# Kernel optimization log

Measured on AMD Instinct MI355X. Metric: run time of the kernel, lower is better.

Reference implementation:

```python
import jax, jax.numpy as jnp
import numpy as np

E = 8   # num_experts
K = 2   # experts per token


def setup_inputs() -> dict:
    key = jax.random.key(0)
    k1, k2, k3, k4 = jax.random.split(key, 4)
    B, S, H, F = 8, 2048, 1024, 2048
    x = jax.random.normal(k1, (B, S, H), jnp.float32)
    Wg = jax.random.normal(k2, (H, E), jnp.float32) * 0.02
    W1 = jax.random.normal(k3, (E, H, F), jnp.float32) * 0.02
    W2 = jax.random.normal(k4, (E, F, H), jnp.float32) * 0.02
    return {"x": x, "Wg": Wg, "W1": W1, "W2": W2}


def reference(x, Wg, W1, W2):
    orig_shape = x.shape
    xt = x.reshape(-1, orig_shape[-1])          # [T, H]
    T = xt.shape[0]

    # router (no jitter noise: training=False path)
    router_logits = xt @ Wg                     # [T, E]
    routing_weights = jax.nn.softmax(router_logits, axis=-1)
    expert_weights, expert_indices = jax.lax.top_k(routing_weights, K)  # [T, K]

    # router z-loss (float32, as in source)
    log_z = jax.nn.logsumexp(router_logits.astype(jnp.float32), axis=-1)
    z_loss = jnp.sum(log_z * log_z) / T

    # load-balancing loss, faithful to source: num_experts taken from
    # router_probs.shape[-1] == K, and one_hot(expert_indices, K)
    # (out-of-range indices -> zero rows under jax.nn.one_hot semantics)
    oh_k = jax.nn.one_hot(expert_indices, K, dtype=jnp.float32)  # [T, K, K]
    expert_mask = jnp.max(oh_k, axis=-2)                          # [T, K]
    tokens_per_expert = jnp.mean(expert_mask, axis=0)             # [K]
    router_prob_per_expert = jnp.mean(expert_weights.astype(jnp.float32), axis=0)  # [K]
    aux_loss = jnp.mean(tokens_per_expert * router_prob_per_expert) * (K ** 2)

    # combine weight per (token, expert): sum of top-k weights routed to e
    cw = jnp.einsum('tk,tke->te', expert_weights,
                    jax.nn.one_hot(expert_indices, E, dtype=expert_weights.dtype))  # [T, E]

    # per-expert MLP, weighted combine (loop over small fixed E)
    out = jnp.zeros_like(xt)
    for e in range(E):
        h = jax.nn.gelu(xt @ W1[e], approximate=False)  # [T, F]
        out = out + cw[:, e:e + 1] * (h @ W2[e])        # [T, H]

    return out.reshape(orig_shape), z_loss, aux_loss
```

## Files before the change

kernel.cpp:

```cpp
#include <hip/hip_runtime.h>
#include <math.h>

#define T_TOKENS 16384
#define H_DIM 1024
#define F_DIM 2048
#define E_NUM 8
#define TPR 72
#define TOT_T (2 * TPR)
#define MAX_PAIRS (TOT_T * 256)

typedef __attribute__((ext_vector_type(8))) short bf16x8;
typedef __attribute__((ext_vector_type(4))) float f32x4;
typedef __attribute__((ext_vector_type(4))) unsigned short us4;

struct TopK { int e0, e1; float w0, w1; };

__device__ __forceinline__ unsigned short f2bf(float f) {
  unsigned int u = __float_as_uint(f);
  u = (u + 0x7fffu + ((u >> 16) & 1u)) >> 16;
  return (unsigned short)u;
}

__device__ __forceinline__ float bf2f(unsigned short u) {
  return __uint_as_float(((unsigned int)u) << 16);
}

__device__ __forceinline__ void gload_lds16(const void* g, void* l) {
  __builtin_amdgcn_global_load_lds(
      (const __attribute__((address_space(1))) void*)g,
      (__attribute__((address_space(3))) void*)l, 16, 0, 0);
}

__global__ __launch_bounds__(256) void transpose_cast(
    const float* __restrict__ in, unsigned short* __restrict__ out, int R, int C) {
  __shared__ float tile[64][65];
  int e = blockIdx.z;
  int r0 = blockIdx.y * 64, c0 = blockIdx.x * 64;
  int tid = threadIdx.x;
  const float* src = in + ((size_t)e * R + r0) * C + c0;
#pragma unroll
  for (int p = 0; p < 4; p++) {
    int id = p * 256 + tid;
    int row = id >> 4, c4 = (id & 15) * 4;
    float4 v = *(const float4*)&src[(size_t)row * C + c4];
    tile[row][c4 + 0] = v.x; tile[row][c4 + 1] = v.y;
    tile[row][c4 + 2] = v.z; tile[row][c4 + 3] = v.w;
  }
  __syncthreads();
  unsigned short* dst = out + ((size_t)e * C + c0) * R + r0;
#pragma unroll
  for (int p = 0; p < 4; p++) {
    int id = p * 256 + tid;
    int c = id >> 4, r4 = (id & 15) * 4;
    us4 pk;
#pragma unroll
    for (int j = 0; j < 4; j++) pk[j] = f2bf(tile[r4 + j][c]);
    *(us4*)&dst[(size_t)c * R + r4] = pk;
  }
}

__global__ __launch_bounds__(256) void prep_kernel(
    const float* __restrict__ x, const float* __restrict__ Wg,
    const float* __restrict__ W1, unsigned short* __restrict__ xb,
    unsigned short* __restrict__ w1t, TopK* __restrict__ topk,
    int* __restrict__ counts, float* __restrict__ scal) {
  __shared__ __align__(16) char shraw[E_NUM * H_DIM * 4 + 256];
  int bid = blockIdx.x;
  int tid = threadIdx.x;
  if (bid >= 1024) {
    float* tile = (float*)shraw;
    int lb = bid - 1024;
    int bx = lb & 31, by = (lb >> 5) & 15, e = lb >> 9;
    int r0 = by * 64, c0 = bx * 64;
    const float* src = W1 + ((size_t)e * H_DIM + r0) * F_DIM + c0;
#pragma unroll
    for (int p = 0; p < 4; p++) {
      int id = p * 256 + tid;
      int row = id >> 4, c4 = (id & 15) * 4;
      float4 v = *(const float4*)&src[(size_t)row * F_DIM + c4];
      tile[row * 65 + c4 + 0] = v.x; tile[row * 65 + c4 + 1] = v.y;
      tile[row * 65 + c4 + 2] = v.z; tile[row * 65 + c4 + 3] = v.w;
    }
    __syncthreads();
    unsigned short* dst = w1t + ((size_t)e * F_DIM + c0) * H_DIM + r0;
#pragma unroll
    for (int p = 0; p < 4; p++) {
      int id = p * 256 + tid;
      int c = id >> 4, r4 = (id & 15) * 4;
      us4 pk;
#pragma unroll
      for (int j = 0; j < 4; j++) pk[j] = f2bf(tile[(r4 + j) * 65 + c]);
      *(us4*)&dst[(size_t)c * H_DIM + r4] = pk;
    }
    return;
  }
  float (*wg)[H_DIM] = (float(*)[H_DIM])shraw;
  int* cnt = (int*)(shraw + E_NUM * H_DIM * 4);
  float (*sred)[5] = (float(*)[5])(shraw + E_NUM * H_DIM * 4 + 64);
  if (tid < 16) cnt[tid] = 0;
  for (int i = tid; i < E_NUM * H_DIM; i += 256) wg[i & 7][i >> 3] = Wg[i];
  __syncthreads();
  int lane = tid & 63, wid = tid >> 6;
  float zacc = 0.f, c0 = 0.f, c1 = 0.f, s0 = 0.f, s1 = 0.f;
  int wgid = bid * 4 + wid;
#pragma unroll
  for (int it = 0; it < 4; ++it) {
    int t = wgid + it * 4096;
    const float4* xr = (const float4*)(x + (size_t)t * H_DIM);
    us4* xbr = (us4*)(xb + (size_t)t * H_DIM);
    float l[E_NUM];
#pragma unroll
    for (int e = 0; e < E_NUM; e++) l[e] = 0.f;
#pragma unroll
    for (int i = 0; i < 4; i++) {
      int j = i * 64 + lane;
      float4 v = xr[j];
      us4 pk;
      pk[0] = f2bf(v.x); pk[1] = f2bf(v.y); pk[2] = f2bf(v.z); pk[3] = f2bf(v.w);
      xbr[j] = pk;
      int h = j * 4;
#pragma unroll
      for (int e = 0; e < E_NUM; e++) {
        const f32x4 wv = *(const f32x4*)&wg[e][h];
        l[e] = fmaf(v.x, wv[0], l[e]);
        l[e] = fmaf(v.y, wv[1], l[e]);
        l[e] = fmaf(v.z, wv[2], l[e]);
        l[e] = fmaf(v.w, wv[3], l[e]);
      }
    }
#pragma unroll
    for (int off = 32; off > 0; off >>= 1) {
#pragma unroll
      for (int e = 0; e < E_NUM; e++) l[e] += __shfl_xor(l[e], off, 64);
    }
    if (lane == 0) {
      float mx = l[0];
#pragma unroll
      for (int e = 1; e < E_NUM; e++) mx = fmaxf(mx, l[e]);
      float p[E_NUM]; float se = 0.f;
#pragma unroll
      for (int e = 0; e < E_NUM; e++) { p[e] = expf(l[e] - mx); se += p[e]; }
      float logz = logf(se) + mx;
      int e0 = 0; float b0 = p[0];
#pragma unroll
      for (int e = 1; e < E_NUM; e++) if (p[e] > b0) { b0 = p[e]; e0 = e; }
      int e1 = -1; float b1 = -1.f;
#pragma unroll
      for (int e = 0; e < E_NUM; e++) if (e != e0 && p[e] > b1) { b1 = p[e]; e1 = e; }
      float w0 = b0 / se, w1 = b1 / se;
      TopK tk; tk.e0 = e0; tk.e1 = e1; tk.w0 = w0; tk.w1 = w1;
      topk[t] = tk;
      atomicAdd(&cnt[e0], 1);
      atomicAdd(&cnt[8 + e1], 1);
      zacc += logz * logz;
      c0 += (e0 == 0 || e1 == 0) ? 1.f : 0.f;
      c1 += (e0 == 1 || e1 == 1) ? 1.f : 0.f;
      s0 += w0; s1 += w1;
    }
  }
  if (lane == 0) {
    sred[wid][0] = zacc; sred[wid][1] = c0; sred[wid][2] = c1;
    sred[wid][3] = s0;   sred[wid][4] = s1;
  }
  __syncthreads();
  if (tid == 0) {
    float a[5] = {0.f, 0.f, 0.f, 0.f, 0.f};
    for (int w2 = 0; w2 < 4; w2++)
      for (int k = 0; k < 5; k++) a[k] += sred[w2][k];
    for (int k = 0; k < 5; k++) atomicAdd(&scal[k], a[k]);
  }
  if (tid < 16 && cnt[tid]) atomicAdd(&counts[tid], cnt[tid]);
}

__global__ __launch_bounds__(256) void scan_kernel(
    const int* __restrict__ counts, int* __restrict__ po,
    int* __restrict__ tile_expert) {
  __shared__ int nt[16], start[16];
  int tid = threadIdx.x;
  if (tid < 16) {
    int r = tid >> 3, e = tid & 7;
    int s = 0;
    for (int j = 0; j < e; j++) s += (counts[(r << 3) + j] + 255) >> 8;
    nt[tid] = (counts[tid] + 255) >> 8;
    start[tid] = s;
    po[tid] = r * TPR * 256 + (s << 8);
  }
  __syncthreads();
  for (int ti = tid; ti < TOT_T; ti += 256) {
    int r = ti / TPR, local = ti % TPR;
    int ex = -1;
#pragma unroll
    for (int e = 0; e < E_NUM; e++) {
      int k = (r << 3) + e;
      if (local >= start[k] && local < start[k] + nt[k]) ex = e;
    }
    tile_expert[ti] = ex;
  }
}

__global__ __launch_bounds__(256) void assign_kernel(
    const TopK* __restrict__ topk, const int* __restrict__ po,
    int* __restrict__ cursors, int* __restrict__ pair_token,
    float* __restrict__ pair_w, int* __restrict__ inv0, int* __restrict__ inv1) {
  __shared__ int lcnt[16], lbase[16];
  int tid = threadIdx.x;
  if (tid < 16) lcnt[tid] = 0;
  __syncthreads();
  int t = blockIdx.x * 256 + tid;
  TopK tk = topk[t];
  int li0 = atomicAdd(&lcnt[tk.e0], 1);
  int li1 = atomicAdd(&lcnt[8 + tk.e1], 1);
  __syncthreads();
  if (tid < 16) lbase[tid] = lcnt[tid] ? atomicAdd(&cursors[tid], lcnt[tid]) : 0;
  __syncthreads();
  int p0 = po[tk.e0] + lbase[tk.e0] + li0;
  pair_token[p0] = t; pair_w[p0] = tk.w0; inv0[t] = p0;
  int p1 = po[8 + tk.e1] + lbase[8 + tk.e1] + li1;
  pair_token[p1] = t; pair_w[p1] = tk.w1; inv1[t] = p1;
}

template <int MODE, int K, int N, int NTILES>
__global__ __launch_bounds__(512) void moe_gemm8(
    const unsigned short* __restrict__ A, const unsigned short* __restrict__ Bt,
    const int* __restrict__ pair_token, const float* __restrict__ pair_w,
    const int* __restrict__ tile_expert, int tile_base,
    unsigned short* __restrict__ outbf) {
  constexpr int NBN = N / 256;
  constexpr int NTk = K / 64;
  constexpr int MTC = NTILES / 8;
  constexpr int OSTRIDE = (MODE == 0) ? N : K;
  int l = blockIdx.x;
  int xcd = l & 7, idx = l >> 3;
  int mt = tile_base + xcd * MTC + idx / NBN;
  int nb = idx % NBN;
  int e = tile_expert[mt];
  if (e < 0) return;
  int m0 = mt << 8, n0 = nb << 8;

  extern __shared__ __align__(16) char smem_raw[];
  unsigned short* lds = (unsigned short*)smem_raw;

  int tid = threadIdx.x, lane = tid & 63, wid = tid >> 6;
  int wm = wid >> 2, wn = wid & 3;
  int lo = lane & 15, hi = lane >> 4;
  int l7 = lane & 7;

  int aRB = (wm * 64 + lo) * 64;
  int bRB = (wn * 32 + lo) * 64;
  int kd0 = (hi ^ l7) * 8;
  int kd1 = ((4 + hi) ^ l7) * 8;

  int kcs = ((tid & 7) ^ ((tid >> 3) & 7)) * 8;
  int rr = tid >> 3;
  const unsigned short *aSrc[2][2], *bSrc[2][2];
#pragma unroll
  for (int qa = 0; qa < 2; qa++)
#pragma unroll
    for (int j = 0; j < 2; j++) {
      int row = j * 128 + qa * 64 + rr;
      size_t off;
      if (MODE == 0) {
        int tk = pair_token[m0 + row]; if (tk < 0) tk = 0;
        off = (size_t)tk * K;
      } else {
        off = (size_t)(m0 + row) * K;
      }
      aSrc[qa][j] = A + off + kcs;
    }
#pragma unroll
  for (int qb = 0; qb < 2; qb++)
#pragma unroll
    for (int j = 0; j < 2; j++) {
      int rp = j * 64 + rr;
      int col = (rp >> 5) * 64 + qb * 32 + (rp & 31);
      bSrc[qb][j] = Bt + ((size_t)e * N + n0 + col) * K + kcs;
    }

#define ST_A(qa, s, sb) do { if ((s) < NTk) { \
    gload_lds16(aSrc[qa][0] + (size_t)(s) * 64, lds + (sb) + (qa) * 8192 + wid * 512); \
    gload_lds16(aSrc[qa][1] + (size_t)(s) * 64, lds + (sb) + (qa) * 8192 + 4096 + wid * 512); } } while (0)
#define ST_B(qb, s, sb) do { if ((s) < NTk) { \
    gload_lds16(bSrc[qb][0] + (size_t)(s) * 64, lds + (sb) + 16384 + (qb) * 8192 + wid * 512); \
    gload_lds16(bSrc[qb][1] + (size_t)(s) * 64, lds + (sb) + 16384 + (qb) * 8192 + 4096 + wid * 512); } } while (0)
#define RD_A(dst, qa, rb) do { _Pragma("unroll") \
    for (int mf = 0; mf < 4; mf++) { \
      dst[mf * 2 + 0] = *(const bf16x8*)&lds[(rb) + (qa) * 8192 + aRB + mf * 1024 + kd0]; \
      dst[mf * 2 + 1] = *(const bf16x8*)&lds[(rb) + (qa) * 8192 + aRB + mf * 1024 + kd1]; } } while (0)
#define RD_B(dst, qb, rb) do { _Pragma("unroll") \
    for (int nf = 0; nf < 2; nf++) { \
      dst[nf * 2 + 0] = *(const bf16x8*)&lds[(rb) + 16384 + (qb) * 8192 + bRB + nf * 1024 + kd0]; \
      dst[nf * 2 + 1] = *(const bf16x8*)&lds[(rb) + 16384 + (qb) * 8192 + bRB + nf * 1024 + kd1]; } } while (0)
#define MMQ(aq, bq, QA, QB) do { __builtin_amdgcn_s_setprio(1); _Pragma("unroll") \
    for (int mf = 0; mf < 4; mf++) _Pragma("unroll") \
    for (int nf = 0; nf < 2; nf++) { \
      acc[(QA) * 4 + mf][(QB) * 2 + nf] = __builtin_amdgcn_mfma_f32_16x16x32_bf16( \
          bq[nf * 2 + 0], aq[mf * 2 + 0], acc[(QA) * 4 + mf][(QB) * 2 + nf], 0, 0, 0); \
      acc[(QA) * 4 + mf][(QB) * 2 + nf] = __builtin_amdgcn_mfma_f32_16x16x32_bf16( \
          bq[nf * 2 + 1], aq[mf * 2 + 1], acc[(QA) * 4 + mf][(QB) * 2 + nf], 0, 0, 0); } \
    __builtin_amdgcn_s_setprio(0); } while (0)
#define PH_BAR() do { asm volatile("s_barrier" ::: "memory"); \
    __builtin_amdgcn_sched_barrier(0); } while (0)
#define VMC(n) do { asm volatile("s_waitcnt vmcnt(" #n ")" ::: "memory"); \
    __builtin_amdgcn_sched_barrier(0); } while (0)

  f32x4 acc[8][4];
#pragma unroll
  for (int i = 0; i < 8; i++)
#pragma unroll
    for (int j = 0; j < 4; j++) acc[i][j] = (f32x4){0.f, 0.f, 0.f, 0.f};

  bf16x8 afr[8], bfr0[4], bfr1[4];

  ST_A(0, 0, 0); ST_B(0, 0, 0); ST_B(1, 0, 0); ST_A(1, 0, 0);
  ST_A(0, 1, 32768); ST_B(0, 1, 32768);
  VMC(4); PH_BAR();

  for (int t = 0; t < NTk; ++t) {
    int bo = (t & 1) << 15, bn = bo ^ 32768;
    RD_A(afr, 0, bo);
    RD_B(bfr0, 0, bo);
    ST_B(1, t + 1, bn);
    VMC(8); PH_BAR();
    MMQ(afr, bfr0, 0, 0);
    RD_B(bfr1, 1, bo);
    ST_A(1, t + 1, bn);
    PH_BAR();
    MMQ(afr, bfr1, 0, 1);
    RD_A(afr, 1, bo);
    ST_A(0, t + 2, bo);
    VMC(8); PH_BAR();
    MMQ(afr, bfr1, 1, 1);
    ST_B(0, t + 2, bo);
    PH_BAR();
    MMQ(afr, bfr0, 1, 0);
  }
  asm volatile("s_waitcnt vmcnt(0)" ::: "memory");
  __builtin_amdgcn_sched_barrier(0);
#undef ST_A
#undef ST_B
#undef RD_A
#undef RD_B
#undef MMQ
#undef PH_BAR
#undef VMC

#pragma unroll
  for (int mh = 0; mh < 2; mh++)
#pragma unroll
    for (int mf = 0; mf < 4; mf++) {
      size_t p = m0 + wm * 128 + mh * 64 + mf * 16 + lo;
      float w = (MODE == 0) ? 0.f : pair_w[p];
#pragma unroll
      for (int nf = 0; nf < 4; nf++) {
        int f = n0 + wn * 64 + nf * 16 + hi * 4;
        us4 pk;
#pragma unroll
        for (int r = 0; r < 4; r++) {
          float v = acc[mh * 4 + mf][nf][r];
          if (MODE == 0) {
            float u = fmaf(0.044715f * v * v, v, v);
            float s = 1.f / (1.f + __expf(-1.5957691216057308f * u));
            pk[r] = f2bf(v * s);
          } else {
            pk[r] = f2bf(w * v);
          }
        }
        *(us4*)&outbf[p * (size_t)OSTRIDE + f] = pk;
      }
    }
}

__global__ __launch_bounds__(256) void combine_kernel(
    const unsigned short* __restrict__ hout, const int* __restrict__ inv0,
    const int* __restrict__ inv1, float* __restrict__ outp,
    const float* __restrict__ scal) {
  int idx = blockIdx.x * 256 + threadIdx.x;
  int t = idx >> 7;
  int c = (idx & 127) * 8;
  int p0 = inv0[t], p1 = inv1[t];
  bf16x8 va = *(const bf16x8*)&hout[(size_t)p0 * F_DIM + c];
  bf16x8 vb = *(const bf16x8*)&hout[(size_t)p1 * F_DIM + c];
  float* orow = outp + (size_t)t * H_DIM + c;
  float4 o0, o1;
  o0.x = bf2f((unsigned short)va[0]) + bf2f((unsigned short)vb[0]);
  o0.y = bf2f((unsigned short)va[1]) + bf2f((unsigned short)vb[1]);
  o0.z = bf2f((unsigned short)va[2]) + bf2f((unsigned short)vb[2]);
  o0.w = bf2f((unsigned short)va[3]) + bf2f((unsigned short)vb[3]);
  o1.x = bf2f((unsigned short)va[4]) + bf2f((unsigned short)vb[4]);
  o1.y = bf2f((unsigned short)va[5]) + bf2f((unsigned short)vb[5]);
  o1.z = bf2f((unsigned short)va[6]) + bf2f((unsigned short)vb[6]);
  o1.w = bf2f((unsigned short)va[7]) + bf2f((unsigned short)vb[7]);
  *(float4*)&orow[0] = o0;
  *(float4*)&orow[4] = o1;
  if (idx == 0) {
    float invT = 1.f / (float)T_TOKENS;
    float* outTail = outp + (size_t)T_TOKENS * H_DIM;
    outTail[0] = scal[0] * invT;
    float tpe0 = scal[1] * invT, tpe1 = scal[2] * invT;
    float rp0 = scal[3] * invT, rp1 = scal[4] * invT;
    outTail[1] = (tpe0 * rp0 + tpe1 * rp1) * 0.5f * 4.f;
  }
}

extern "C" void kernel_launch(void* const* d_in, const int* in_sizes, int n_in,
                              void* d_out, int out_size, void* d_ws, size_t ws_size,
                              hipStream_t stream) {
  const float* x  = (const float*)d_in[0];
  const float* Wg = (const float*)d_in[1];
  const float* W1 = (const float*)d_in[2];
  const float* W2 = (const float*)d_in[3];
  float* outp = (float*)d_out;

  char* w = (char*)d_ws;
  auto alloc = [&](size_t b) { char* p = w; w += (b + 511) & ~(size_t)511; return p; };
  char*  meta        = alloc(256);
  float* scal        = (float*)(meta + 0);
  int*   counts      = (int*)(meta + 64);
  int*   cursors     = (int*)(meta + 128);
  int*   po          = (int*)alloc(64);
  int*   tile_expert = (int*)alloc(TOT_T * 4);
  TopK*  topk        = (TopK*)alloc((size_t)T_TOKENS * sizeof(TopK));
  int*   pair_token  = (int*)alloc((size_t)MAX_PAIRS * 4);
  float* pair_w      = (float*)alloc((size_t)MAX_PAIRS * 4);
  int*   inv0        = (int*)alloc((size_t)T_TOKENS * 4);
  int*   inv1        = (int*)alloc((size_t)T_TOKENS * 4);
  unsigned short* xb   = (unsigned short*)alloc((size_t)T_TOKENS * H_DIM * 2 + 512);
  unsigned short* w1t  = (unsigned short*)alloc((size_t)E_NUM * F_DIM * H_DIM * 2 + 512);
  unsigned short* hmid = (unsigned short*)alloc((size_t)MAX_PAIRS * F_DIM * 2 + 512);
  unsigned short* w2t = xb;

  hipFuncSetAttribute((const void*)&moe_gemm8<0, H_DIM, F_DIM, TOT_T>,
                      hipFuncAttributeMaxDynamicSharedMemorySize, 131072);
  hipFuncSetAttribute((const void*)&moe_gemm8<1, F_DIM, H_DIM, TOT_T>,
                      hipFuncAttributeMaxDynamicSharedMemorySize, 131072);

  hipMemsetAsync(meta, 0, 256, stream);
  hipMemsetAsync(pair_token, 0xFF, (size_t)MAX_PAIRS * 4, stream);

  dim3 b256(256), b512(512);
  prep_kernel<<<dim3(5120), b256, 0, stream>>>(x, Wg, W1, xb, w1t, topk, counts, scal);
  scan_kernel<<<1, b256, 0, stream>>>(counts, po, tile_expert);
  assign_kernel<<<T_TOKENS / 256, b256, 0, stream>>>(topk, po, cursors, pair_token, pair_w,
                                                     inv0, inv1);
  moe_gemm8<0, H_DIM, F_DIM, TOT_T><<<dim3((F_DIM / 256) * TOT_T), b512, 131072, stream>>>(
      xb, w1t, pair_token, pair_w, tile_expert, 0, hmid);
  transpose_cast<<<dim3(H_DIM / 64, F_DIM / 64, E_NUM), b256, 0, stream>>>(W2, w2t, F_DIM, H_DIM);
  moe_gemm8<1, F_DIM, H_DIM, TOT_T><<<dim3((H_DIM / 256) * TOT_T), b512, 131072, stream>>>(
      hmid, w2t, pair_token, pair_w, tile_expert, 0, hmid);
  combine_kernel<<<dim3(T_TOKENS * 128 / 256), b256, 0, stream>>>(hmid, inv0, inv1, outp, scal);
}
```

Before: 484.0 us.

## Fold W2 transpose-cast into prep kernel and use incrementing load pointers

The separate W2 transpose/bf16-cast launch is merged into the prep kernel as extra blocks. Its output now goes into the output buffer as scratch instead of aliasing xb, which had forced it to run after the first GEMM. The GEMM mainloop now advances precomputed source pointers per stage instead of recomputing addresses, and unrolls by two. The aim is to cut one launch, let the W2 conversion overlap with routing work, and lower address arithmetic in the hot loop. In exchange, prep does more work up front and d_out must not be needed before combine, which now overwrites it.

```diff
diff --git a/kernel.cpp b/kernel.cpp
--- a/kernel.cpp
+++ b/kernel.cpp
@@ -31,11 +31,10 @@
       (__attribute__((address_space(3))) void*)l, 16, 0, 0);
 }
 
-__global__ __launch_bounds__(256) void transpose_cast(
-    const float* __restrict__ in, unsigned short* __restrict__ out, int R, int C) {
-  __shared__ float tile[64][65];
-  int e = blockIdx.z;
-  int r0 = blockIdx.y * 64, c0 = blockIdx.x * 64;
+__device__ __forceinline__ void transpose_body(
+    const float* __restrict__ in, unsigned short* __restrict__ out,
+    int R, int C, int bx, int by, int e, float* tile ) {
+  int r0 = by * 64, c0 = bx * 64;
   int tid = threadIdx.x;
   const float* src = in + ((size_t)e * R + r0) * C + c0;
 #pragma unroll
@@ -43,8 +42,8 @@
     int id = p * 256 + tid;
     int row = id >> 4, c4 = (id & 15) * 4;
     float4 v = *(const float4*)&src[(size_t)row * C + c4];
-    tile[row][c4 + 0] = v.x; tile[row][c4 + 1] = v.y;
-    tile[row][c4 + 2] = v.z; tile[row][c4 + 3] = v.w;
+    tile[row * 65 + c4 + 0] = v.x; tile[row * 65 + c4 + 1] = v.y;
+    tile[row * 65 + c4 + 2] = v.z; tile[row * 65 + c4 + 3] = v.w;
   }
   __syncthreads();
   unsigned short* dst = out + ((size_t)e * C + c0) * R + r0;
@@ -54,43 +53,28 @@
     int c = id >> 4, r4 = (id & 15) * 4;
     us4 pk;
 #pragma unroll
-    for (int j = 0; j < 4; j++) pk[j] = f2bf(tile[r4 + j][c]);
+    for (int j = 0; j < 4; j++) pk[j] = f2bf(tile[(r4 + j) * 65 + c]);
     *(us4*)&dst[(size_t)c * R + r4] = pk;
   }
 }
 
 __global__ __launch_bounds__(256) void prep_kernel(
     const float* __restrict__ x, const float* __restrict__ Wg,
-    const float* __restrict__ W1, unsigned short* __restrict__ xb,
-    unsigned short* __restrict__ w1t, TopK* __restrict__ topk,
+    const float* __restrict__ W1, const float* __restrict__ W2,
+    unsigned short* __restrict__ xb, unsigned short* __restrict__ w1t,
+    unsigned short* __restrict__ w2t, TopK* __restrict__ topk,
     int* __restrict__ counts, float* __restrict__ scal) {
   __shared__ __align__(16) char shraw[E_NUM * H_DIM * 4 + 256];
   int bid = blockIdx.x;
   int tid = threadIdx.x;
   if (bid >= 1024) {
     float* tile = (float*)shraw;
-    int lb = bid - 1024;
-    int bx = lb & 31, by = (lb >> 5) & 15, e = lb >> 9;
-    int r0 = by * 64, c0 = bx * 64;
-    const float* src = W1 + ((size_t)e * H_DIM + r0) * F_DIM + c0;
-#pragma unroll
-    for (int p = 0; p < 4; p++) {
-      int id = p * 256 + tid;
-      int row = id >> 4, c4 = (id & 15) * 4;
-      float4 v = *(const float4*)&src[(size_t)row * F_DIM + c4];
-      tile[row * 65 + c4 + 0] = v.x; tile[row * 65 + c4 + 1] = v.y;
-      tile[row * 65 + c4 + 2] = v.z; tile[row * 65 + c4 + 3] = v.w;
-    }
-    __syncthreads();
-    unsigned short* dst = w1t + ((size_t)e * F_DIM + c0) * H_DIM + r0;
-#pragma unroll
-    for (int p = 0; p < 4; p++) {
-      int id = p * 256 + tid;
-      int c = id >> 4, r4 = (id & 15) * 4;
-      us4 pk;
-#pragma unroll
-      for (int j = 0; j < 4; j++) pk[j] = f2bf(tile[(r4 + j) * 65 + c]);
-      *(us4*)&dst[(size_t)c * H_DIM + r4] = pk;
+    if (bid < 5120) {
+      int lb = bid - 1024;
+      transpose_body(W1, w1t, H_DIM, F_DIM, lb & 31, (lb >> 5) & 15, lb >> 9, tile);
+    } else {
+      int lb = bid - 5120;
+      transpose_body(W2, w2t, F_DIM, H_DIM, lb & 15, (lb >> 4) & 31, lb >> 9, tile);
     }
     return;
   }
@@ -276,12 +260,13 @@
       bSrc[qb][j] = Bt + ((size_t)e * N + n0 + col) * K + kcs;
     }
 
-#define ST_A(qa, s, sb) do { if ((s) < NTk) { \
-    gload_lds16(aSrc[qa][0] + (size_t)(s) * 64, lds + (sb) + (qa) * 8192 + wid * 512); \
-    gload_lds16(aSrc[qa][1] + (size_t)(s) * 64, lds + (sb) + (qa) * 8192 + 4096 + wid * 512); } } while (0)
-#define ST_B(qb, s, sb) do { if ((s) < NTk) { \
-    gload_lds16(bSrc[qb][0] + (size_t)(s) * 64, lds + (sb) + 16384 + (qb) * 8192 + wid * 512); \
-    gload_lds16(bSrc[qb][1] + (size_t)(s) * 64, lds + (sb) + 16384 + (qb) * 8192 + 4096 + wid * 512); } } while (0)
+#define ST0(src, qa, s, sb) do { \
+    gload_lds16(src[qa][0] + (size_t)(s) * 64, lds + (sb) + wid * 512); \
+    gload_lds16(src[qa][1] + (size_t)(s) * 64, lds + (sb) + 4096 + wid * 512); } while (0)
+#define ST_P(ptr, base, g) do { if (g) { \
+    gload_lds16(ptr[0], lds + (base) + wid * 512); \
+    gload_lds16(ptr[1], lds + (base) + 4096 + wid * 512); \
+    ptr[0] += 64; ptr[1] += 64; } } while (0)
 #define RD_A(dst, qa, rb) do { _Pragma("unroll") \
     for (int mf = 0; mf < 4; mf++) { \
       dst[mf * 2 + 0] = *(const bf16x8*)&lds[(rb) + (qa) * 8192 + aRB + mf * 1024 + kd0]; \
@@ -311,33 +296,40 @@
 
   bf16x8 afr[8], bfr0[4], bfr1[4];
 
-  ST_A(0, 0, 0); ST_B(0, 0, 0); ST_B(1, 0, 0); ST_A(1, 0, 0);
-  ST_A(0, 1, 32768); ST_B(0, 1, 32768);
+  ST0(aSrc, 0, 0, 0); ST0(bSrc, 0, 0, 16384); ST0(bSrc, 1, 0, 24576); ST0(aSrc, 1, 0, 8192);
+  ST0(aSrc, 0, 1, 32768); ST0(bSrc, 0, 1, 32768 + 16384);
   VMC(4); PH_BAR();
 
+  const unsigned short* pB1[2] = {bSrc[1][0] + 64, bSrc[1][1] + 64};
+  const unsigned short* pA1[2] = {aSrc[1][0] + 64, aSrc[1][1] + 64};
+  const unsigned short* pA0[2] = {aSrc[0][0] + 128, aSrc[0][1] + 128};
+  const unsigned short* pB0[2] = {bSrc[0][0] + 128, bSrc[0][1] + 128};
+
+#pragma unroll 2
   for (int t = 0; t < NTk; ++t) {
     int bo = (t & 1) << 15, bn = bo ^ 32768;
+    bool g1 = (t + 1 < NTk), g2 = (t + 2 < NTk);
     RD_A(afr, 0, bo);
     RD_B(bfr0, 0, bo);
-    ST_B(1, t + 1, bn);
+    ST_P(pB1, bn + 24576, g1);
     VMC(8); PH_BAR();
     MMQ(afr, bfr0, 0, 0);
     RD_B(bfr1, 1, bo);
-    ST_A(1, t + 1, bn);
+    ST_P(pA1, bn + 8192, g1);
     PH_BAR();
     MMQ(afr, bfr1, 0, 1);
     RD_A(afr, 1, bo);
-    ST_A(0, t + 2, bo);
+    ST_P(pA0, bo, g2);
     VMC(8); PH_BAR();
     MMQ(afr, bfr1, 1, 1);
-    ST_B(0, t + 2, bo);
+    ST_P(pB0, bo + 16384, g2);
     PH_BAR();
     MMQ(afr, bfr0, 1, 0);
   }
   asm volatile("s_waitcnt vmcnt(0)" ::: "memory");
   __builtin_amdgcn_sched_barrier(0);
-#undef ST_A
-#undef ST_B
+#undef ST0
+#undef ST_P
 #undef RD_A
 #undef RD_B
 #undef MMQ
@@ -427,7 +419,7 @@
   unsigned short* xb   = (unsigned short*)alloc((size_t)T_TOKENS * H_DIM * 2 + 512);
   unsigned short* w1t  = (unsigned short*)alloc((size_t)E_NUM * F_DIM * H_DIM * 2 + 512);
   unsigned short* hmid = (unsigned short*)alloc((size_t)MAX_PAIRS * F_DIM * 2 + 512);
-  unsigned short* w2t = xb;
+  unsigned short* w2t = (unsigned short*)d_out;
 
   hipFuncSetAttribute((const void*)&moe_gemm8<0, H_DIM, F_DIM, TOT_T>,
                       hipFuncAttributeMaxDynamicSharedMemorySize, 131072);
@@ -438,13 +430,13 @@
   hipMemsetAsync(pair_token, 0xFF, (size_t)MAX_PAIRS * 4, stream);
 
   dim3 b256(256), b512(512);
-  prep_kernel<<<dim3(5120), b256, 0, stream>>>(x, Wg, W1, xb, w1t, topk, counts, scal);
+  prep_kernel<<<dim3(9216), b256, 0, stream>>>(x, Wg, W1, W2, xb, w1t, w2t,
+                                               topk, counts, scal);
   scan_kernel<<<1, b256, 0, stream>>>(counts, po, tile_expert);
   assign_kernel<<<T_TOKENS / 256, b256, 0, stream>>>(topk, po, cursors, pair_token, pair_w,
                                                      inv0, inv1);
   moe_gemm8<0, H_DIM, F_DIM, TOT_T><<<dim3((F_DIM / 256) * TOT_T), b512, 131072, stream>>>(
       xb, w1t, pair_token, pair_w, tile_expert, 0, hmid);
-  transpose_cast<<<dim3(H_DIM / 64, F_DIM / 64, E_NUM), b256, 0, stream>>>(W2, w2t, F_DIM, H_DIM);
   moe_gemm8<1, F_DIM, H_DIM, TOT_T><<<dim3((H_DIM / 256) * TOT_T), b512, 131072, stream>>>(
       hmid, w2t, pair_token, pair_w, tile_expert, 0, hmid);
   combine_kernel<<<dim3(T_TOKENS * 128 / 256), b256, 0, stream>>>(hmid, inv0, inv1, outp, scal);
```

Result: faster. 472.1 us (-2.5%).
